# Kernel optimization log

Hardware: AMD Instinct MI355X
Metric: run time of the kernel (lower is better)

## Reference

```python
import jax, jax.numpy as jnp
import numpy as np

BATCH = 65536
IN_FEATURES = 128
OUT_FEATURES = 128
GRID = 8  # initial_grid: number of RBF/spline basis centers per edge


def setup_inputs() -> dict:
    key = jax.random.key(0)
    k1, k2, k3 = jax.random.split(key, 3)
    x = jax.random.normal(k1, (BATCH, IN_FEATURES), dtype=jnp.float32)
    # Per-edge spline coefficients stacked: [out, in, grid]
    coeffs = jax.random.normal(k2, (OUT_FEATURES, IN_FEATURES, GRID), dtype=jnp.float32) * 0.1
    # Per-edge base (SiLU) weights stacked: [out, in]
    base_w = jax.random.normal(k3, (OUT_FEATURES, IN_FEATURES), dtype=jnp.float32) * 0.1
    # Shared uniform grid of RBF centers in [-1, 1]
    centers = jnp.linspace(-1.0, 1.0, GRID, dtype=jnp.float32)
    return {"x": x, "coeffs": coeffs, "base_w": base_w, "centers": centers}


def reference(x, coeffs, base_w, centers):
    # HybridBasisFunction per edge: base_w * silu(x) + sum_g coeffs[g] * exp(-((x-c_g)/w)^2)
    width = 2.0 / (GRID - 1)  # grid spacing
    # basis: [B, in, G]
    diff = (x[:, :, None] - centers[None, None, :]) / width
    basis = jnp.exp(-diff * diff)
    # Sum over all edges (j -> i): output[b, i] = sum_j phi_ij(x[b, j])
    out = jnp.einsum('big,oig->bo', basis, coeffs)
    out = out + jnp.einsum('bi,oi->bo', jax.nn.silu(x), base_w)
    return out
```

## Files before the change

### kernel.cpp

```cpp
#include <hip/hip_runtime.h>

typedef _Float16 f16x8 __attribute__((ext_vector_type(8)));
typedef float    f32x4 __attribute__((ext_vector_type(4)));

#define BATCH 65536
#define NIN   128
#define NOUT  128
#define NKS   36

#define AS  4.2039284307525743f
#define L2E 1.4426950408889634f


__global__ __launch_bounds__(256) void kan_prep(const float* __restrict__ coeffs,
                                                const float* __restrict__ base_w,
                                                _Float16* __restrict__ W2) {
    int t = blockIdx.x * 256 + threadIdx.x;
    int ks  = t >> 9;
    int c   = t & 511;
    int nb  = c >> 6;
    int l15 = (c >> 2) & 15;
    int lhi = c & 3;
    int n     = nb * 16 + l15;
    int kslot = ks * 4 + lhi;
    f16x8 v;
    if (kslot < 128) {
        const float* src = coeffs + ((size_t)n * 128 + kslot) * 8;
#pragma unroll
        for (int e = 0; e < 8; ++e) v[e] = (_Float16)src[e];
    } else {
        const float* src = base_w + (size_t)n * 128 + (size_t)(kslot - 128) * 8;
#pragma unroll
        for (int e = 0; e < 8; ++e) v[e] = (_Float16)src[e];
    }
    *(f16x8*)((char*)W2 + (size_t)t * 16) = v;
}

__device__ __forceinline__ void gll16(const void* g, void* l) {
    __builtin_amdgcn_global_load_lds(
        (const __attribute__((address_space(1))) unsigned int*)g,
        (__attribute__((address_space(3))) unsigned int*)l, 16, 0, 0);
}

__device__ __forceinline__ f16x8 basis8(float xv, const float* bq) {
    f16x8 r;
#pragma unroll
    for (int g = 0; g < 8; ++g) {
        float u = __builtin_fmaf(xv, AS, bq[g]);
        float e = __builtin_amdgcn_exp2f(-(u * u));
        r[g] = (_Float16)e;
    }
    return r;
}

__device__ __forceinline__ float silu1(float xv) {
    float p = __builtin_amdgcn_exp2f(-xv * L2E);
    return xv * __builtin_amdgcn_rcpf(1.0f + p);
}

__global__ __launch_bounds__(256) void kan_main(const float* __restrict__ x,
                                                const float* __restrict__ centers,
                                                const _Float16* __restrict__ W2,
                                                float* __restrict__ out) {
    __shared__ _Float16 smem[2][4096];

    const int tid  = threadIdx.x;
    const int lane = tid & 63;
    const int wave = tid >> 6;
    const int l15  = lane & 15;
    const int lhi  = lane >> 4;
    const int row0 = blockIdx.x * 128 + wave * 32;

    float bq[8];
#pragma unroll
    for (int g = 0; g < 8; ++g) bq[g] = -centers[g] * AS;

    const float* xrow = x + (size_t)(row0 + l15) * NIN;

    f32x4 acc[2][8];
#pragma unroll
    for (int m = 0; m < 2; ++m)
#pragma unroll
        for (int nb = 0; nb < 8; ++nb) acc[m][nb] = (f32x4){0.f, 0.f, 0.f, 0.f};

    const char* w2base = (const char*)W2;
#define STAGE(buf, ks)                                                          \
    do {                                                                        \
        const char* _s = w2base + (size_t)(ks) * 8192 + (size_t)tid * 16;       \
        gll16(_s,        (char*)&smem[(buf)][0]    + tid * 16);                 \
        gll16(_s + 4096, (char*)&smem[(buf)][2048] + tid * 16);                 \
    } while (0)

    STAGE(0, 0);
    __syncthreads();

#pragma unroll 2
    for (int ks = 0; ks < 32; ++ks) {
        const int cur = ks & 1;
        STAGE(cur ^ 1, ks + 1);
        f16x8 a0 = basis8(xrow[ks * 4 + lhi], bq);
        f16x8 a1 = basis8(xrow[2048 + ks * 4 + lhi], bq);
        const _Float16* bp = &smem[cur][(size_t)l15 * 32 + lhi * 8];
#pragma unroll
        for (int nb = 0; nb < 8; ++nb) {
            f16x8 b = *(const f16x8*)(bp + nb * 512);
            acc[0][nb] = __builtin_amdgcn_mfma_f32_16x16x32_f16(a0, b, acc[0][nb], 0, 0, 0);
            acc[1][nb] = __builtin_amdgcn_mfma_f32_16x16x32_f16(a1, b, acc[1][nb], 0, 0, 0);
        }
        __syncthreads();
    }

#pragma unroll 2
    for (int ks = 32; ks < NKS; ++ks) {
        const int cur = ks & 1;
        if (ks + 1 < NKS) STAGE(cur ^ 1, ks + 1);
        f16x8 a[2];
#pragma unroll
        for (int m = 0; m < 2; ++m) {
            const float* xp = xrow + m * 2048 + (ks - 32) * 32 + lhi * 8;
            f32x4 v0 = *(const f32x4*)xp;
            f32x4 v1 = *(const f32x4*)(xp + 4);
#pragma unroll
            for (int e = 0; e < 4; ++e) a[m][e]     = (_Float16)silu1(v0[e]);
#pragma unroll
            for (int e = 0; e < 4; ++e) a[m][4 + e] = (_Float16)silu1(v1[e]);
        }
        const _Float16* bp = &smem[cur][(size_t)l15 * 32 + lhi * 8];
#pragma unroll
        for (int nb = 0; nb < 8; ++nb) {
            f16x8 b = *(const f16x8*)(bp + nb * 512);
            acc[0][nb] = __builtin_amdgcn_mfma_f32_16x16x32_f16(a[0], b, acc[0][nb], 0, 0, 0);
            acc[1][nb] = __builtin_amdgcn_mfma_f32_16x16x32_f16(a[1], b, acc[1][nb], 0, 0, 0);
        }
        __syncthreads();
    }

#pragma unroll
    for (int m = 0; m < 2; ++m)
#pragma unroll
        for (int nb = 0; nb < 8; ++nb)
#pragma unroll
            for (int r = 0; r < 4; ++r)
                out[(size_t)(row0 + m * 16 + lhi * 4 + r) * NOUT + nb * 16 + l15] = acc[m][nb][r];
}

extern "C" void kernel_launch(void* const* d_in, const int* in_sizes, int n_in,
                              void* d_out, int out_size, void* d_ws, size_t ws_size,
                              hipStream_t stream) {
    const float* x       = (const float*)d_in[0];
    const float* coeffs  = (const float*)d_in[1];
    const float* base_w  = (const float*)d_in[2];
    const float* centers = (const float*)d_in[3];
    _Float16* W2 = (_Float16*)d_ws;

    kan_prep<<<dim3(72), dim3(256), 0, stream>>>(coeffs, base_w, W2);
    kan_main<<<dim3(BATCH / 128), dim3(256), 0, stream>>>(x, centers, W2, (float*)d_out);
}
```

Before: 45.59 us.

## Widen per-wave M tile to 64 rows and stage larger weight chunks

Blocks drop to two waves, each computing 64 rows (4 M-tiles) so every B fragment read from LDS feeds four MFMAs instead of two. The weight prep is re-laid out so each lane's K slice is contiguous in x, which allows vectorized f32x4 x loads prefetched one group ahead. Weights are staged in 32KB chunks over 8 iterations instead of 36 small steps, which cuts barrier count. The cost is more accumulator registers (128 floats), 64KB of LDS per block and fewer waves per block, so occupancy and latency hiding may drop.

Result: slower. 48.10 us (+5.5%).

```diff
diff --git a/kernel.cpp b/kernel.cpp
--- a/kernel.cpp
+++ b/kernel.cpp
@@ -6,7 +6,6 @@
 #define BATCH 65536
 #define NIN   128
 #define NOUT  128
-#define NKS   36
 
 #define AS  4.2039284307525743f
 #define L2E 1.4426950408889634f
@@ -16,23 +15,19 @@
                                                 const float* __restrict__ base_w,
                                                 _Float16* __restrict__ W2) {
     int t = blockIdx.x * 256 + threadIdx.x;
-    int ks  = t >> 9;
-    int c   = t & 511;
-    int nb  = c >> 6;
-    int l15 = (c >> 2) & 15;
-    int lhi = c & 3;
-    int n     = nb * 16 + l15;
-    int kslot = ks * 4 + lhi;
+    int ks   = t >> 9;
+    int c    = t & 511;
+    int nb   = c >> 6;
+    int lane = c & 63;
+    int lhi  = lane >> 4;
+    int l15  = lane & 15;
+    int n    = nb * 16 + l15;
+    const float* src;
+    if (ks < 32) src = coeffs + ((size_t)n * 128 + lhi * 32 + ks) * 8;
+    else         src = base_w + (size_t)n * 128 + lhi * 32 + (ks - 32) * 8;
     f16x8 v;
-    if (kslot < 128) {
-        const float* src = coeffs + ((size_t)n * 128 + kslot) * 8;
 #pragma unroll
-        for (int e = 0; e < 8; ++e) v[e] = (_Float16)src[e];
-    } else {
-        const float* src = base_w + (size_t)n * 128 + (size_t)(kslot - 128) * 8;
-#pragma unroll
-        for (int e = 0; e < 8; ++e) v[e] = (_Float16)src[e];
-    }
+    for (int e = 0; e < 8; ++e) v[e] = (_Float16)src[e];
     *(f16x8*)((char*)W2 + (size_t)t * 16) = v;
 }
 
@@ -58,85 +53,98 @@
     return xv * __builtin_amdgcn_rcpf(1.0f + p);
 }
 
-__global__ __launch_bounds__(256) void kan_main(const float* __restrict__ x,
+__global__ __launch_bounds__(128) void kan_main(const float* __restrict__ x,
                                                 const float* __restrict__ centers,
                                                 const _Float16* __restrict__ W2,
                                                 float* __restrict__ out) {
-    __shared__ _Float16 smem[2][4096];
+    __shared__ _Float16 smem[2][16384];
 
     const int tid  = threadIdx.x;
     const int lane = tid & 63;
-    const int wave = tid >> 6;
+    const int w    = tid >> 6;
     const int l15  = lane & 15;
     const int lhi  = lane >> 4;
-    const int row0 = blockIdx.x * 128 + wave * 32;
+    const int row0 = blockIdx.x * 128 + w * 64;
 
     float bq[8];
 #pragma unroll
     for (int g = 0; g < 8; ++g) bq[g] = -centers[g] * AS;
 
-    const float* xrow = x + (size_t)(row0 + l15) * NIN;
+    const float* xp = x + (size_t)(row0 + l15) * NIN + lhi * 32;
 
-    f32x4 acc[2][8];
+    f32x4 acc[4][8];
 #pragma unroll
-    for (int m = 0; m < 2; ++m)
+    for (int m = 0; m < 4; ++m)
 #pragma unroll
         for (int nb = 0; nb < 8; ++nb) acc[m][nb] = (f32x4){0.f, 0.f, 0.f, 0.f};
 
     const char* w2base = (const char*)W2;
-#define STAGE(buf, ks)                                                          \
+#define STAGE(buf, grp)                                                         \
     do {                                                                        \
-        const char* _s = w2base + (size_t)(ks) * 8192 + (size_t)tid * 16;       \
-        gll16(_s,        (char*)&smem[(buf)][0]    + tid * 16);                 \
-        gll16(_s + 4096, (char*)&smem[(buf)][2048] + tid * 16);                 \
+        const char* _s = w2base + (size_t)(grp) * 32768 + (size_t)tid * 16;     \
+        char*       _d = (char*)&smem[(buf)][0] + (size_t)tid * 16;             \
+        _Pragma("unroll")                                                       \
+        for (int _i = 0; _i < 16; ++_i) gll16(_s + _i * 2048, _d + _i * 2048);  \
     } while (0)
 
     STAGE(0, 0);
+    f32x4 xq[4];
+#pragma unroll
+    for (int m = 0; m < 4; ++m) xq[m] = *(const f32x4*)(xp + m * 2048);
     __syncthreads();
 
 #pragma unroll 2
-    for (int ks = 0; ks < 32; ++ks) {
-        const int cur = ks & 1;
-        STAGE(cur ^ 1, ks + 1);
-        f16x8 a0 = basis8(xrow[ks * 4 + lhi], bq);
-        f16x8 a1 = basis8(xrow[2048 + ks * 4 + lhi], bq);
-        const _Float16* bp = &smem[cur][(size_t)l15 * 32 + lhi * 8];
+    for (int g = 0; g < 8; ++g) {
+        const int cur = g & 1;
+        STAGE(cur ^ 1, g + 1);
+        f32x4 xn[4];
+        if (g < 7) {
 #pragma unroll
-        for (int nb = 0; nb < 8; ++nb) {
-            f16x8 b = *(const f16x8*)(bp + nb * 512);
-            acc[0][nb] = __builtin_amdgcn_mfma_f32_16x16x32_f16(a0, b, acc[0][nb], 0, 0, 0);
-            acc[1][nb] = __builtin_amdgcn_mfma_f32_16x16x32_f16(a1, b, acc[1][nb], 0, 0, 0);
+            for (int m = 0; m < 4; ++m) xn[m] = *(const f32x4*)(xp + m * 2048 + (g + 1) * 4);
         }
-        __syncthreads();
-    }
-
-#pragma unroll 2
-    for (int ks = 32; ks < NKS; ++ks) {
-        const int cur = ks & 1;
-        if (ks + 1 < NKS) STAGE(cur ^ 1, ks + 1);
-        f16x8 a[2];
 #pragma unroll
-        for (int m = 0; m < 2; ++m) {
-            const float* xp = xrow + m * 2048 + (ks - 32) * 32 + lhi * 8;
-            f32x4 v0 = *(const f32x4*)xp;
-            f32x4 v1 = *(const f32x4*)(xp + 4);
+        for (int t2 = 0; t2 < 4; ++t2) {
+            f16x8 a[4];
 #pragma unroll
-            for (int e = 0; e < 4; ++e) a[m][e]     = (_Float16)silu1(v0[e]);
+            for (int m = 0; m < 4; ++m) a[m] = basis8(xq[m][t2], bq);
+            const _Float16* bp = &smem[cur][t2 * 4096 + lane * 8];
 #pragma unroll
-            for (int e = 0; e < 4; ++e) a[m][4 + e] = (_Float16)silu1(v1[e]);
+            for (int nb = 0; nb < 8; ++nb) {
+                f16x8 b = *(const f16x8*)(bp + nb * 512);
+#pragma unroll
+                for (int m = 0; m < 4; ++m)
+                    acc[m][nb] = __builtin_amdgcn_mfma_f32_16x16x32_f16(a[m], b, acc[m][nb], 0, 0, 0);
+            }
         }
-        const _Float16* bp = &smem[cur][(size_t)l15 * 32 + lhi * 8];
+        if (g < 7) {
 #pragma unroll
-        for (int nb = 0; nb < 8; ++nb) {
-            f16x8 b = *(const f16x8*)(bp + nb * 512);
-            acc[0][nb] = __builtin_amdgcn_mfma_f32_16x16x32_f16(a[0], b, acc[0][nb], 0, 0, 0);
-            acc[1][nb] = __builtin_amdgcn_mfma_f32_16x16x32_f16(a[1], b, acc[1][nb], 0, 0, 0);
+            for (int m = 0; m < 4; ++m) xq[m] = xn[m];
         }
         __syncthreads();
     }
 
 #pragma unroll
-    for (int m = 0; m < 2; ++m)
+    for (int t2 = 0; t2 < 4; ++t2) {
+        f16x8 a[4];
+#pragma unroll
+        for (int m = 0; m < 4; ++m) {
+            f32x4 v0 = *(const f32x4*)(xp + m * 2048 + t2 * 8);
+            f32x4 v1 = *(const f32x4*)(xp + m * 2048 + t2 * 8 + 4);
+#pragma unroll
+            for (int e = 0; e < 4; ++e) { a[m][e] = (_Float16)silu1(v0[e]); a[m][4 + e] = (_Float16)silu1(v1[e]); }
+        }
+        const _Float16* bp = &smem[0][t2 * 4096 + lane * 8];
+#pragma unroll
+        for (int nb = 0; nb < 8; ++nb) {
+            f16x8 b = *(const f16x8*)(bp + nb * 512);
+#pragma unroll
+            for (int m = 0; m < 4; ++m)
+                acc[m][nb] = __builtin_amdgcn_mfma_f32_16x16x32_f16(a[m], b, acc[m][nb], 0, 0, 0);
+        }
+    }
+
+#pragma unroll
+    for (int m = 0; m < 4; ++m)
 #pragma unroll
         for (int nb = 0; nb < 8; ++nb)
 #pragma unroll
@@ -154,5 +162,5 @@
     _Float16* W2 = (_Float16*)d_ws;
 
     kan_prep<<<dim3(72), dim3(256), 0, stream>>>(coeffs, base_w, W2);
-    kan_main<<<dim3(BATCH / 128), dim3(256), 0, stream>>>(x, centers, W2, (float*)d_out);
+    kan_main<<<dim3(BATCH / 128), dim3(128), 0, stream>>>(x, centers, W2, (float*)d_out);
 }
```
